# Optimization experiments

Measured on AMD Instinct MI355X. Metric: run time of the kernel, lower is better.

Reference implementation:

```python
import jax, jax.numpy as jnp
import numpy as np

WEIGHT_THRESH = 0.5
EPS = 1e-5


def setup_inputs() -> dict:
    key = jax.random.key(0)
    k1, k2, k3 = jax.random.split(key, 3)
    B, N = 2048, 4096
    src_points = jax.random.normal(k1, (B, N, 3), dtype=jnp.float32)
    tgt_points = jax.random.normal(k2, (B, N, 3), dtype=jnp.float32)
    weights = jax.random.uniform(k3, (B, N), dtype=jnp.float32)
    return {"src_points": src_points, "tgt_points": tgt_points, "weights": weights}


def reference(src_points, tgt_points, weights):
    # threshold + normalize weights  (B, N)
    w = jnp.where(weights < WEIGHT_THRESH, jnp.zeros_like(weights), weights)
    w = w / (jnp.sum(w, axis=1, keepdims=True) + EPS)
    w = w[:, :, None]  # (B, N, 1)

    # weighted centroids (B, 1, 3)
    src_centroid = jnp.sum(src_points * w, axis=1, keepdims=True)
    ref_centroid = jnp.sum(tgt_points * w, axis=1, keepdims=True)

    src_c = src_points - src_centroid
    ref_c = tgt_points - ref_centroid

    # weighted 3x3 covariance H = src_c^T @ (ref_c * w)   (B, 3, 3)
    H = jnp.einsum('bni,bnj->bij', src_c, ref_c * w)

    # Kabsch: tf.linalg.svd returns S, U, V (V not transposed); jnp returns U, S, Vh
    U, S, Vh = jnp.linalg.svd(H)
    V = jnp.swapaxes(Vh, -1, -2)
    Ut = jnp.swapaxes(U, -1, -2)
    det = jnp.linalg.det(jnp.matmul(V, Ut))  # (B,)

    ones = jnp.ones_like(det)
    d = jnp.stack([ones, ones, jnp.sign(det)], axis=-1)  # (B, 3) diag of sign-fix eye
    R = jnp.matmul(V * d[:, None, :], Ut)  # V @ diag(d) @ U^T  (B, 3, 3)

    t = ref_centroid[:, 0, :] - jnp.einsum('bij,bj->bi', R, src_centroid[:, 0, :])  # (B, 3)
    return R, t
```

## Files before the change

kernel.cpp:

```cpp
#include <hip/hip_runtime.h>
#include <math.h>

#define BATCH   2048
#define NPTS    4096
#define THREADS 256
#define CHUNKS  4
#define CPTS    (NPTS / CHUNKS)
#define WTHRESH 0.5f
#define EPS     1e-5

__device__ __forceinline__ void async_ld16(const void* g, void* l) {
  __builtin_amdgcn_global_load_lds((const __attribute__((address_space(1))) void*)g,
                                   (__attribute__((address_space(3))) void*)l, 16, 0, 0);
}

__device__ __forceinline__ void reduce_block16(float* acc, float* red ) {
#pragma unroll
  for (int off = 32; off > 0; off >>= 1) {
#pragma unroll
    for (int i = 0; i < 16; ++i) acc[i] += __shfl_down(acc[i], off, 64);
  }
  const int wave = threadIdx.x >> 6;
  const int lane = threadIdx.x & 63;
  if (lane == 0) {
#pragma unroll
    for (int i = 0; i < 16; ++i) red[wave * 16 + i] = acc[i];
  }
  __syncthreads();
  if (threadIdx.x == 0) {
#pragma unroll
    for (int w = 1; w < 4; ++w)
#pragma unroll
      for (int i = 0; i < 16; ++i) acc[i] += red[w * 16 + i];
  }
}

__device__ __forceinline__ void accum_pts(float4 w4, float4 s0, float4 s1, float4 s2,
                                          float4 r0, float4 r1, float4 r2, float* acc) {
  float ww[4] = {w4.x, w4.y, w4.z, w4.w};
  float ps[4][3] = {{s0.x, s0.y, s0.z}, {s0.w, s1.x, s1.y},
                    {s1.z, s1.w, s2.x}, {s2.y, s2.z, s2.w}};
  float qs[4][3] = {{r0.x, r0.y, r0.z}, {r0.w, r1.x, r1.y},
                    {r1.z, r1.w, r2.x}, {r2.y, r2.z, r2.w}};
#pragma unroll
  for (int i = 0; i < 4; ++i) {
    float w = (ww[i] < WTHRESH) ? 0.f : ww[i];
    acc[0] += w;
    float wp0 = w * ps[i][0], wp1 = w * ps[i][1], wp2 = w * ps[i][2];
    acc[1] += wp0; acc[2] += wp1; acc[3] += wp2;
    acc[4] += w * qs[i][0]; acc[5] += w * qs[i][1]; acc[6] += w * qs[i][2];
    acc[7]  += wp0 * qs[i][0]; acc[8]  += wp0 * qs[i][1]; acc[9]  += wp0 * qs[i][2];
    acc[10] += wp1 * qs[i][0]; acc[11] += wp1 * qs[i][1]; acc[12] += wp1 * qs[i][2];
    acc[13] += wp2 * qs[i][0]; acc[14] += wp2 * qs[i][1]; acc[15] += wp2 * qs[i][2];
  }
}


#define JROT(app, aqq, apq, apt, aqt, vp0, vq0, vp1, vq1, vp2, vq2)            \
  {                                                                            \
    bool go = fabs(apq) > 1e-300;                                              \
    double apq_s = go ? apq : 1.0;                                             \
    double theta = (aqq - app) / (2.0 * apq_s);                                \
    double tt = copysign(1.0, theta) / (fabs(theta) + sqrt(theta*theta + 1.0));\
    double cc = 1.0 / sqrt(tt*tt + 1.0);                                       \
    double ss = tt * cc;                                                       \
    cc = go ? cc : 1.0; ss = go ? ss : 0.0;                                    \
    double app_n = cc*cc*app - 2.0*cc*ss*apq + ss*ss*aqq;                      \
    double aqq_n = ss*ss*app + 2.0*cc*ss*apq + cc*cc*aqq;                      \
    double apt_n = cc*apt - ss*aqt;                                            \
    double aqt_n = ss*apt + cc*aqt;                                            \
    app = app_n; aqq = aqq_n; apq = 0.0; apt = apt_n; aqt = aqt_n;             \
    double tv;                                                                 \
    tv = vp0; vp0 = cc*tv - ss*vq0; vq0 = ss*tv + cc*vq0;                      \
    tv = vp1; vp1 = cc*tv - ss*vq1; vq1 = ss*tv + cc*vq1;                      \
    tv = vp2; vp2 = cc*tv - ss*vq2; vq2 = ss*tv + cc*vq2;                      \
  }

#define CSWAP(ea, eb, x0, y0, x1, y1, x2, y2)                                  \
  { bool sw = ea < eb; double td;                                              \
    td = ea; ea = sw ? eb : ea; eb = sw ? td : eb;                             \
    td = x0; x0 = sw ? y0 : x0; y0 = sw ? td : y0;                             \
    td = x1; x1 = sw ? y1 : x1; y1 = sw ? td : y1;                             \
    td = x2; x2 = sw ? y2 : x2; y2 = sw ? td : y2; }

__device__ void solve_from_acc(const float* acc, float* R9, float* t3) {
  const double W = acc[0];
  const double inv = 1.0 / (W + EPS);
  const double sc0 = acc[1] * inv, sc1 = acc[2] * inv, sc2 = acc[3] * inv;
  const double tc0 = acc[4] * inv, tc1 = acc[5] * inv, tc2 = acc[6] * inv;
  const double f = 2.0 - W * inv;

  const double h00 = acc[7]  * inv - sc0 * tc0 * f;
  const double h01 = acc[8]  * inv - sc0 * tc1 * f;
  const double h02 = acc[9]  * inv - sc0 * tc2 * f;
  const double h10 = acc[10] * inv - sc1 * tc0 * f;
  const double h11 = acc[11] * inv - sc1 * tc1 * f;
  const double h12 = acc[12] * inv - sc1 * tc2 * f;
  const double h20 = acc[13] * inv - sc2 * tc0 * f;
  const double h21 = acc[14] * inv - sc2 * tc1 * f;
  const double h22 = acc[15] * inv - sc2 * tc2 * f;

  double a00 = h00*h00 + h10*h10 + h20*h20;
  double a01 = h00*h01 + h10*h11 + h20*h21;
  double a02 = h00*h02 + h10*h12 + h20*h22;
  double a11 = h01*h01 + h11*h11 + h21*h21;
  double a12 = h01*h02 + h11*h12 + h21*h22;
  double a22 = h02*h02 + h12*h12 + h22*h22;

  double v00 = 1, v01 = 0, v02 = 0;
  double v10 = 0, v11 = 1, v12 = 0;
  double v20 = 0, v21 = 0, v22 = 1;

  for (int sweep = 0; sweep < 7; ++sweep) {
    JROT(a00, a11, a01, a02, a12, v00, v01, v10, v11, v20, v21)
    JROT(a00, a22, a02, a01, a12, v00, v02, v10, v12, v20, v22)
    JROT(a11, a22, a12, a01, a02, v01, v02, v11, v12, v21, v22)
  }

  double e0 = a00, e1 = a11, e2 = a22;
  CSWAP(e0, e1, v00, v01, v10, v11, v20, v21)
  CSWAP(e0, e2, v00, v02, v10, v12, v20, v22)
  CSWAP(e1, e2, v01, v02, v11, v12, v21, v22)

  double u1x = h00*v00 + h01*v10 + h02*v20;
  double u1y = h10*v00 + h11*v10 + h12*v20;
  double u1z = h20*v00 + h21*v10 + h22*v20;
  double n1 = sqrt(u1x*u1x + u1y*u1y + u1z*u1z);
  bool ok1 = n1 > 1e-150;
  double r1 = 1.0 / n1;
  u1x = ok1 ? u1x * r1 : 1.0;
  u1y = ok1 ? u1y * r1 : 0.0;
  u1z = ok1 ? u1z * r1 : 0.0;

  double u2x = h00*v01 + h01*v11 + h02*v21;
  double u2y = h10*v01 + h11*v11 + h12*v21;
  double u2z = h20*v01 + h21*v11 + h22*v21;
  double d12 = u1x*u2x + u1y*u2y + u1z*u2z;
  u2x -= d12 * u1x; u2y -= d12 * u1y; u2z -= d12 * u1z;
  double n2 = sqrt(u2x*u2x + u2y*u2y + u2z*u2z);
  bool ok2 = n2 > 1e-150;
  double fx = (fabs(u1x) < 0.9) ? 1.0 : 0.0;
  double fy = 1.0 - fx;
  double dd = fx*u1x + fy*u1y;
  double gx = fx - dd*u1x, gy = fy - dd*u1y, gz = -dd*u1z;
  double rg = 1.0 / sqrt(gx*gx + gy*gy + gz*gz);
  double r2 = 1.0 / n2;
  u2x = ok2 ? u2x * r2 : gx * rg;
  u2y = ok2 ? u2y * r2 : gy * rg;
  u2z = ok2 ? u2z * r2 : gz * rg;

  double w3x = u1y*u2z - u1z*u2y;
  double w3y = u1z*u2x - u1x*u2z;
  double w3z = u1x*u2y - u1y*u2x;

  double cxx = v11*v22 - v21*v12;
  double cxy = v21*v02 - v01*v22;
  double cxz = v01*v12 - v11*v02;
  double dv = v00*cxx + v10*cxy + v20*cxz;
  dv = (dv >= 0.0) ? 1.0 : -1.0;

  double R00 = v00*u1x + v01*u2x + dv*v02*w3x;
  double R01 = v00*u1y + v01*u2y + dv*v02*w3y;
  double R02 = v00*u1z + v01*u2z + dv*v02*w3z;
  double R10 = v10*u1x + v11*u2x + dv*v12*w3x;
  double R11 = v10*u1y + v11*u2y + dv*v12*w3y;
  double R12 = v10*u1z + v11*u2z + dv*v12*w3z;
  double R20 = v20*u1x + v21*u2x + dv*v22*w3x;
  double R21 = v20*u1y + v21*u2y + dv*v22*w3y;
  double R22 = v20*u1z + v21*u2z + dv*v22*w3z;

  R9[0] = (float)R00; R9[1] = (float)R01; R9[2] = (float)R02;
  R9[3] = (float)R10; R9[4] = (float)R11; R9[5] = (float)R12;
  R9[6] = (float)R20; R9[7] = (float)R21; R9[8] = (float)R22;
  t3[0] = (float)(tc0 - (R00*sc0 + R01*sc1 + R02*sc2));
  t3[1] = (float)(tc1 - (R10*sc0 + R11*sc1 + R12*sc2));
  t3[2] = (float)(tc2 - (R20*sc0 + R21*sc1 + R22*sc2));
}

__global__ __launch_bounds__(THREADS) void wp_reduce_lds(const float* __restrict__ src,
                                                         const float* __restrict__ tgt,
                                                         const float* __restrict__ wts,
                                                         float* __restrict__ partials) {
  __shared__ float4 lds_w[CPTS / 4];
  __shared__ float4 lds_s[CPTS * 3 / 4];
  __shared__ float4 lds_t[CPTS * 3 / 4];
  __shared__ float red[64];

  const int bid = blockIdx.x;
  const int b = bid >> 2;
  const int c = bid & 3;
  const size_t poff = (size_t)b * NPTS + (size_t)c * CPTS;
  const float4* gw = (const float4*)(wts + poff);
  const float4* gs = (const float4*)(src + poff * 3);
  const float4* gt = (const float4*)(tgt + poff * 3);

  const int t = threadIdx.x;
  async_ld16(gw + t, lds_w + t);
#pragma unroll
  for (int k = 0; k < 3; ++k) async_ld16(gs + t + k * THREADS, lds_s + t + k * THREADS);
#pragma unroll
  for (int k = 0; k < 3; ++k) async_ld16(gt + t + k * THREADS, lds_t + t + k * THREADS);

  asm volatile("s_waitcnt vmcnt(0)" ::: "memory");
  __syncthreads();

  float4 w4 = lds_w[t];
  float4 s0 = lds_s[t * 3], s1 = lds_s[t * 3 + 1], s2 = lds_s[t * 3 + 2];
  float4 r0 = lds_t[t * 3], r1 = lds_t[t * 3 + 1], r2 = lds_t[t * 3 + 2];

  float acc[16];
#pragma unroll
  for (int i = 0; i < 16; ++i) acc[i] = 0.f;
  accum_pts(w4, s0, s1, s2, r0, r1, r2, acc);

  reduce_block16(acc, red);
  if (t == 0) {
#pragma unroll
    for (int i = 0; i < 16; ++i) partials[(size_t)bid * 16 + i] = acc[i];
  }
}

__global__ __launch_bounds__(64) void wp_solve(const float* __restrict__ partials,
                                               float* __restrict__ out) {
  const int b = blockIdx.x * 64 + threadIdx.x;
  if (b >= BATCH) return;
  float acc[16];
#pragma unroll
  for (int i = 0; i < 16; ++i) acc[i] = 0.f;
#pragma unroll
  for (int cch = 0; cch < CHUNKS; ++cch)
#pragma unroll
    for (int i = 0; i < 16; ++i)
      acc[i] += partials[(size_t)(b * CHUNKS + cch) * 16 + i];
  float R9[9], t3[3];
  solve_from_acc(acc, R9, t3);
#pragma unroll
  for (int i = 0; i < 9; ++i) out[(size_t)b * 9 + i] = R9[i];
#pragma unroll
  for (int i = 0; i < 3; ++i) out[(size_t)BATCH * 9 + (size_t)b * 3 + i] = t3[i];
}

__global__ __launch_bounds__(THREADS) void wp_fused(const float* __restrict__ src,
                                                    const float* __restrict__ tgt,
                                                    const float* __restrict__ wts,
                                                    float* __restrict__ out) {
  __shared__ float red[64];
  const int b = blockIdx.x;
  float acc[16];
#pragma unroll
  for (int i = 0; i < 16; ++i) acc[i] = 0.f;
  for (int c = 0; c < CHUNKS; ++c) {
    const size_t poff = (size_t)b * NPTS + (size_t)c * CPTS;
    const int p0 = threadIdx.x * 4;
    float4 w4 = *(const float4*)(wts + poff + p0);
    const float4* sp = (const float4*)(src + (poff + p0) * 3);
    const float4* tp = (const float4*)(tgt + (poff + p0) * 3);
    accum_pts(w4, sp[0], sp[1], sp[2], tp[0], tp[1], tp[2], acc);
  }
  reduce_block16(acc, red);
  if (threadIdx.x == 0) {
    float R9[9], t3[3];
    solve_from_acc(acc, R9, t3);
#pragma unroll
    for (int i = 0; i < 9; ++i) out[(size_t)b * 9 + i] = R9[i];
#pragma unroll
    for (int i = 0; i < 3; ++i) out[(size_t)BATCH * 9 + (size_t)b * 3 + i] = t3[i];
  }
}

extern "C" void kernel_launch(void* const* d_in, const int* in_sizes, int n_in,
                              void* d_out, int out_size, void* d_ws, size_t ws_size,
                              hipStream_t stream) {
  const float* src = (const float*)d_in[0];
  const float* tgt = (const float*)d_in[1];
  const float* wts = (const float*)d_in[2];
  float* out = (float*)d_out;

  if (ws_size >= (size_t)BATCH * CHUNKS * 16 * sizeof(float)) {
    float* partials = (float*)d_ws;
    wp_reduce_lds<<<BATCH * CHUNKS, THREADS, 0, stream>>>(src, tgt, wts, partials);
    wp_solve<<<(BATCH + 63) / 64, 64, 0, stream>>>(partials, out);
  } else {
    wp_fused<<<BATCH, THREADS, 0, stream>>>(src, tgt, wts, out);
  }
}
```

Baseline: 245.3 us.

## Replace two-kernel LDS reduction with single fused kernel using nontemporal loads

Drops the split reduce-to-partials plus solve kernels and always runs one fused kernel per batch. Each thread loads its four chunks directly from global memory with nontemporal loads, fully unrolled. Block indices are remapped so each XCD handles a contiguous range of batches. This removes the second launch, the partials round trip and the LDS staging. In exchange there are fewer blocks (2048 instead of 8192), and the SVD solve runs serially on thread 0 of each block, which may leave that tail latency less hidden.

```diff
diff --git a/kernel.cpp b/kernel.cpp
--- a/kernel.cpp
+++ b/kernel.cpp
@@ -4,15 +4,11 @@
 #define BATCH   2048
 #define NPTS    4096
 #define THREADS 256
-#define CHUNKS  4
-#define CPTS    (NPTS / CHUNKS)
+#define NXCD    8
 #define WTHRESH 0.5f
 #define EPS     1e-5
 
-__device__ __forceinline__ void async_ld16(const void* g, void* l) {
-  __builtin_amdgcn_global_load_lds((const __attribute__((address_space(1))) void*)g,
-                                   (__attribute__((address_space(3))) void*)l, 16, 0, 0);
-}
+typedef float f4 __attribute__((ext_vector_type(4)));
 
 __device__ __forceinline__ void reduce_block16(float* acc, float* red ) {
 #pragma unroll
@@ -35,8 +31,8 @@
   }
 }
 
-__device__ __forceinline__ void accum_pts(float4 w4, float4 s0, float4 s1, float4 s2,
-                                          float4 r0, float4 r1, float4 r2, float* acc) {
+__device__ __forceinline__ void accum_pts(f4 w4, f4 s0, f4 s1, f4 s2,
+                                          f4 r0, f4 r1, f4 r2, float* acc) {
   float ww[4] = {w4.x, w4.y, w4.z, w4.w};
   float ps[4][3] = {{s0.x, s0.y, s0.z}, {s0.w, s1.x, s1.y},
                     {s1.z, s1.w, s2.x}, {s2.y, s2.z, s2.w}};
@@ -54,7 +50,6 @@
     acc[13] += wp2 * qs[i][0]; acc[14] += wp2 * qs[i][1]; acc[15] += wp2 * qs[i][2];
   }
 }
-
 
 #define JROT(app, aqq, apq, apt, aqt, vp0, vq0, vp1, vq1, vp2, vq2)            \
   {                                                                            \
@@ -177,88 +172,39 @@
   t3[2] = (float)(tc2 - (R20*sc0 + R21*sc1 + R22*sc2));
 }
 
-__global__ __launch_bounds__(THREADS) void wp_reduce_lds(const float* __restrict__ src,
-                                                         const float* __restrict__ tgt,
-                                                         const float* __restrict__ wts,
-                                                         float* __restrict__ partials) {
-  __shared__ float4 lds_w[CPTS / 4];
-  __shared__ float4 lds_s[CPTS * 3 / 4];
-  __shared__ float4 lds_t[CPTS * 3 / 4];
-  __shared__ float red[64];
-
-  const int bid = blockIdx.x;
-  const int b = bid >> 2;
-  const int c = bid & 3;
-  const size_t poff = (size_t)b * NPTS + (size_t)c * CPTS;
-  const float4* gw = (const float4*)(wts + poff);
-  const float4* gs = (const float4*)(src + poff * 3);
-  const float4* gt = (const float4*)(tgt + poff * 3);
-
-  const int t = threadIdx.x;
-  async_ld16(gw + t, lds_w + t);
-#pragma unroll
-  for (int k = 0; k < 3; ++k) async_ld16(gs + t + k * THREADS, lds_s + t + k * THREADS);
-#pragma unroll
-  for (int k = 0; k < 3; ++k) async_ld16(gt + t + k * THREADS, lds_t + t + k * THREADS);
-
-  asm volatile("s_waitcnt vmcnt(0)" ::: "memory");
-  __syncthreads();
-
-  float4 w4 = lds_w[t];
-  float4 s0 = lds_s[t * 3], s1 = lds_s[t * 3 + 1], s2 = lds_s[t * 3 + 2];
-  float4 r0 = lds_t[t * 3], r1 = lds_t[t * 3 + 1], r2 = lds_t[t * 3 + 2];
-
-  float acc[16];
-#pragma unroll
-  for (int i = 0; i < 16; ++i) acc[i] = 0.f;
-  accum_pts(w4, s0, s1, s2, r0, r1, r2, acc);
-
-  reduce_block16(acc, red);
-  if (t == 0) {
-#pragma unroll
-    for (int i = 0; i < 16; ++i) partials[(size_t)bid * 16 + i] = acc[i];
-  }
-}
-
-__global__ __launch_bounds__(64) void wp_solve(const float* __restrict__ partials,
-                                               float* __restrict__ out) {
-  const int b = blockIdx.x * 64 + threadIdx.x;
-  if (b >= BATCH) return;
-  float acc[16];
-#pragma unroll
-  for (int i = 0; i < 16; ++i) acc[i] = 0.f;
-#pragma unroll
-  for (int cch = 0; cch < CHUNKS; ++cch)
-#pragma unroll
-    for (int i = 0; i < 16; ++i)
-      acc[i] += partials[(size_t)(b * CHUNKS + cch) * 16 + i];
-  float R9[9], t3[3];
-  solve_from_acc(acc, R9, t3);
-#pragma unroll
-  for (int i = 0; i < 9; ++i) out[(size_t)b * 9 + i] = R9[i];
-#pragma unroll
-  for (int i = 0; i < 3; ++i) out[(size_t)BATCH * 9 + (size_t)b * 3 + i] = t3[i];
-}
-
 __global__ __launch_bounds__(THREADS) void wp_fused(const float* __restrict__ src,
                                                     const float* __restrict__ tgt,
                                                     const float* __restrict__ wts,
                                                     float* __restrict__ out) {
   __shared__ float red[64];
-  const int b = blockIdx.x;
+
+  const int bid = blockIdx.x;
+  const int b = (bid & (NXCD - 1)) * (BATCH / NXCD) + (bid >> 3);
+
+  const int t = threadIdx.x;
   float acc[16];
 #pragma unroll
   for (int i = 0; i < 16; ++i) acc[i] = 0.f;
-  for (int c = 0; c < CHUNKS; ++c) {
-    const size_t poff = (size_t)b * NPTS + (size_t)c * CPTS;
-    const int p0 = threadIdx.x * 4;
-    float4 w4 = *(const float4*)(wts + poff + p0);
-    const float4* sp = (const float4*)(src + (poff + p0) * 3);
-    const float4* tp = (const float4*)(tgt + (poff + p0) * 3);
-    accum_pts(w4, sp[0], sp[1], sp[2], tp[0], tp[1], tp[2], acc);
-  }
+
+#pragma unroll
+  for (int c = 0; c < 4; ++c) {
+    const size_t p0 = (size_t)b * NPTS + (size_t)c * 1024 + (size_t)t * 4;
+    const f4* gw = (const f4*)(wts + p0);
+    const f4* gs = (const f4*)(src + p0 * 3);
+    const f4* gt = (const f4*)(tgt + p0 * 3);
+    f4 w4 = __builtin_nontemporal_load(gw);
+    f4 s0 = __builtin_nontemporal_load(gs + 0);
+    f4 s1 = __builtin_nontemporal_load(gs + 1);
+    f4 s2 = __builtin_nontemporal_load(gs + 2);
+    f4 r0 = __builtin_nontemporal_load(gt + 0);
+    f4 r1 = __builtin_nontemporal_load(gt + 1);
+    f4 r2 = __builtin_nontemporal_load(gt + 2);
+    accum_pts(w4, s0, s1, s2, r0, r1, r2, acc);
+  }
+
   reduce_block16(acc, red);
-  if (threadIdx.x == 0) {
+
+  if (t == 0) {
     float R9[9], t3[3];
     solve_from_acc(acc, R9, t3);
 #pragma unroll
@@ -275,12 +221,5 @@
   const float* tgt = (const float*)d_in[1];
   const float* wts = (const float*)d_in[2];
   float* out = (float*)d_out;
-
-  if (ws_size >= (size_t)BATCH * CHUNKS * 16 * sizeof(float)) {
-    float* partials = (float*)d_ws;
-    wp_reduce_lds<<<BATCH * CHUNKS, THREADS, 0, stream>>>(src, tgt, wts, partials);
-    wp_solve<<<(BATCH + 63) / 64, 64, 0, stream>>>(partials, out);
-  } else {
-    wp_fused<<<BATCH, THREADS, 0, stream>>>(src, tgt, wts, out);
-  }
-}
+  wp_fused<<<BATCH, THREADS, 0, stream>>>(src, tgt, wts, out);
+}
```

Result: no change. 244.1 us (-0.5%).
